# Kernel optimization log

Hardware: AMD Instinct MI355X
Metric: run time of the kernel (lower is better)

Reference implementation:

```python
import jax, jax.numpy as jnp
import numpy as np

B, N, D_MODEL = 4, 4096, 1024
N_HEADS, D_HEAD = 16, 64
NB_FEATURES = int(D_HEAD * np.log(D_HEAD))  # 266, performer default
EPS = 1e-4


def _gaussian_orthogonal_matrix(key, m, d):
    """performer-pytorch gaussian_orthogonal_random_matrix, scaling=0."""
    n_blocks = int(np.ceil(m / d))
    keys = jax.random.split(key, n_blocks + 1)
    blocks = []
    for i in range(n_blocks):
        g = jax.random.normal(keys[i], (d, d), jnp.float32)
        q, _ = jnp.linalg.qr(g)
        blocks.append(q.T)
    mat = jnp.concatenate(blocks, axis=0)[:m]  # [m, d]
    multiplier = jnp.linalg.norm(
        jax.random.normal(keys[-1], (m, d), jnp.float32), axis=1)
    return mat * multiplier[:, None]


def setup_inputs() -> dict:
    key = jax.random.key(0)
    ks = jax.random.split(key, 7)
    s = 1.0 / np.sqrt(D_MODEL)
    x = jax.random.normal(ks[0], (B, N, D_MODEL), jnp.float32)
    Wq = jax.random.normal(ks[1], (D_MODEL, D_MODEL), jnp.float32) * s
    Wk = jax.random.normal(ks[2], (D_MODEL, D_MODEL), jnp.float32) * s
    Wv = jax.random.normal(ks[3], (D_MODEL, D_MODEL), jnp.float32) * s
    Wo = jax.random.normal(ks[4], (D_MODEL, D_MODEL), jnp.float32) * s
    bo = jnp.zeros((D_MODEL,), jnp.float32)
    proj = _gaussian_orthogonal_matrix(ks[5], NB_FEATURES, D_HEAD)
    return {"x": x, "Wq": Wq, "Wk": Wk, "Wv": Wv, "Wo": Wo, "bo": bo,
            "proj": proj}


def _softmax_kernel(data, proj, is_query):
    # data: [b, h, n, d]; proj: [m, d]  (FAVOR+ positive random features)
    ratio = proj.shape[0] ** -0.5
    dn = data.shape[-1] ** -0.25  # data_normalizer
    dash = jnp.einsum('bhnd,md->bhnm', data * dn, proj)
    diag = 0.5 * (dn ** 2) * jnp.sum(data * data, axis=-1, keepdims=True)
    if is_query:
        stab = jnp.max(dash, axis=-1, keepdims=True)
    else:
        stab = jnp.max(dash, axis=(-2, -1), keepdims=True)
    return ratio * (jnp.exp(dash - diag - stab) + EPS)


def reference(x, Wq, Wk, Wv, Wo, bo, proj):
    b, n, _ = x.shape

    def split_heads(t):  # [b,n,D] -> [b,h,n,d]
        return t.reshape(b, n, N_HEADS, D_HEAD).transpose(0, 2, 1, 3)

    q = split_heads(x @ Wq)
    k = split_heads(x @ Wk)
    v = split_heads(x @ Wv)

    qp = _softmax_kernel(q, proj, True)   # [b,h,n,m]
    kp = _softmax_kernel(k, proj, False)  # [b,h,n,m]

    # non-causal linear attention
    k_sum = jnp.sum(kp, axis=2)                                # [b,h,m]
    d_inv = 1.0 / jnp.einsum('bhnm,bhm->bhn', qp, k_sum)       # [b,h,n]
    context = jnp.einsum('bhnm,bhnd->bhmd', kp, v)             # [b,h,m,d]
    out = jnp.einsum('bhnm,bhmd,bhn->bhnd', qp, context, d_inv)

    out = out.transpose(0, 2, 1, 3).reshape(b, n, N_HEADS * D_HEAD)
    return out @ Wo + bo
```

## Files before the change

### kernel.cpp

```cpp
#include <hip/hip_runtime.h>
#include <hip/hip_bf16.h>

typedef unsigned short u16;
typedef unsigned int   u32;
typedef __bf16 bf16x8 __attribute__((ext_vector_type(8)));
typedef float  f32x4  __attribute__((ext_vector_type(4)));
typedef unsigned short u16x8 __attribute__((ext_vector_type(8)));

#define B_    4
#define N_    4096
#define BN_   16384
#define DM_   1024
#define H_    16
#define BH_   64
#define M_    266
#define MP_   288
#define DN_    0.35355339059327373f
#define RATIO_ 0.061313933948496574f
#define EPS_   1e-4f

static __device__ __forceinline__ float b2f(u16 u) {
    union { u32 u; float f; } x; x.u = ((u32)u) << 16; return x.f;
}
static __device__ __forceinline__ u16 f2b(float f) {
    union { float f; u32 u; } x; x.f = f;
    u32 r = x.u + 0x7FFFu + ((x.u >> 16) & 1u);
    return (u16)(r >> 16);
}
static __device__ __forceinline__ u32 ford(float f) {
    u32 u = __float_as_uint(f);
    return (u & 0x80000000u) ? ~u : (u | 0x80000000u);
}
static __device__ __forceinline__ float forddec(u32 u) {
    return (u & 0x80000000u) ? __uint_as_float(u & 0x7FFFFFFFu) : __uint_as_float(~u);
}
static __device__ __forceinline__ f32x4 mfma16(bf16x8 a, bf16x8 b, f32x4 c) {
    return __builtin_amdgcn_mfma_f32_16x16x32_bf16(a, b, c, 0, 0, 0);
}
#define GLOAD16(gp, lp) __builtin_amdgcn_global_load_lds( \
    (const __attribute__((address_space(1))) void*)(gp),  \
    (__attribute__((address_space(3))) void*)(lp), 16, 0, 0)

__global__ __launch_bounds__(256) void pack_all(const float* __restrict__ x, u16* __restrict__ xb,
                                                const float* __restrict__ Wq, const float* __restrict__ Wk,
                                                const float* __restrict__ Wv, const float* __restrict__ Wo,
                                                u16* __restrict__ wT,
                                                const float* __restrict__ proj, u16* __restrict__ projb,
                                                u32* __restrict__ stabk) {
    __shared__ float tile[64][65];
    int bid = blockIdx.x, tid = threadIdx.x;
    if (bid < 16384) {
        int i = (bid * 256 + tid) * 4;
        float4 f = *reinterpret_cast<const float4*>(x + i);
        ushort4 o;
        o.x = f2b(f.x); o.y = f2b(f.y); o.z = f2b(f.z); o.w = f2b(f.w);
        *reinterpret_cast<ushort4*>(xb + i) = o;
    } else if (bid < 16384 + 1024) {
        int u = bid - 16384;
        int i0 = (u & 15) * 64;
        int j0 = (u >> 4) * 64;
        const float* src = (j0 < 1024) ? Wq : (j0 < 2048) ? Wk : (j0 < 3072) ? Wv : Wo;
        int jc = j0 & 1023;
        int tr = tid >> 6, tc = tid & 63;
#pragma unroll
        for (int it = 0; it < 16; ++it) {
            int r = it * 4 + tr;
            tile[r][tc] = src[(size_t)(i0 + r) * 1024 + jc + tc];
        }
        __syncthreads();
#pragma unroll
        for (int it = 0; it < 16; ++it) {
            int r = it * 4 + tr;
            wT[(size_t)(j0 + r) * 1024 + i0 + tc] = f2b(tile[tc][r]);
        }
    } else {
        int i = (bid - 17408) * 256 + tid;
        if (i < MP_ * 64) {
            int m = i >> 6;
            projb[i] = (m < M_) ? f2b(proj[i] * DN_) : (u16)0;
        }
        if (i < BH_) stabk[i] = 0u;
    }
}

template<int OUTF32>
__global__ __launch_bounds__(512, 1) void gemm256(const u16* __restrict__ A, const u16* __restrict__ Bt,
                                                  void* __restrict__ C, const float* __restrict__ bias,
                                                  int Ncols, int nby) {
    __shared__ u16 As[2][256 * 64];
    __shared__ u16 Bs[2][256 * 64];
    constexpr int K = 1024, T = 16;
    int tid = threadIdx.x, lane = tid & 63, wid = tid >> 6;
    int wm = wid >> 2, wn = wid & 3;
    int lr = lane & 15, lk8 = (lane >> 4) * 8;
    int nwg = gridDim.x;
    int wg = ((int)blockIdx.x & 7) * (nwg >> 3) + (int)blockIdx.x / 8;
    int u = wg % (8 * nby), pid = wg / (8 * nby);
    size_t r0 = (size_t)(pid * 8 + (u & 7)) * 256;
    size_t c0 = (size_t)(u / 8) * 256;

    auto stage = [&](int t, int h) {
        int buf = t & 1;
        const u16* src = (h < 2) ? (A + r0 * K) : (Bt + c0 * K);
        u16* dst = (h < 2) ? As[buf] : Bs[buf];
        int rbase = (h & 1) * 128;
        int kt = t * 64;
#pragma unroll
        for (int c = 0; c < 2; ++c) {
            int li0 = rbase * 8 + c * 512 + wid * 64;
            int li = li0 + lane;
            int row = li >> 3, kk = (li & 7) * 8;
            int kks = kk ^ ((row & 7) << 3);
            GLOAD16(&src[(size_t)row * K + kt + kks], (char*)dst + (size_t)li0 * 16);
        }
    };
    auto lda = [&](int buf, int mf, int ks) {
        int row = wm * 128 + mf * 16 + lr;
        return *reinterpret_cast<const bf16x8*>(&As[buf][row * 64 + ((ks * 32 + lk8) ^ ((row & 7) << 3))]);
    };
    auto ldb = [&](int buf, int nf, int ks) {
        int row = wn * 64 + nf * 16 + lr;
        return *reinterpret_cast<const bf16x8*>(&Bs[buf][row * 64 + ((ks * 32 + lk8) ^ ((row & 7) << 3))]);
    };

    f32x4 acc[8][4] = {};
    stage(0, 0); stage(0, 1); stage(0, 2); stage(0, 3);
    stage(1, 2); stage(1, 3); stage(1, 0);
    asm volatile("s_waitcnt vmcnt(6)" ::: "memory");
    __builtin_amdgcn_s_barrier();

#pragma unroll 2
    for (int t = 0; t < T; ++t) {
        const int buf = t & 1;
        bf16x8 av[4][2], aw[4][2], bv[4][2];
#pragma unroll
        for (int mf = 0; mf < 4; ++mf) { av[mf][0] = lda(buf, mf, 0); av[mf][1] = lda(buf, mf, 1); }
#pragma unroll
        for (int nf = 0; nf < 4; ++nf) { bv[nf][0] = ldb(buf, nf, 0); bv[nf][1] = ldb(buf, nf, 1); }
        if (t + 1 < T) stage(t + 1, 1);
        __builtin_amdgcn_s_barrier();
        __builtin_amdgcn_s_setprio(1);
#pragma unroll
        for (int mf = 0; mf < 4; ++mf)
#pragma unroll
            for (int nf = 0; nf < 4; ++nf) {
                acc[mf][nf] = mfma16(av[mf][0], bv[nf][0], acc[mf][nf]);
                acc[mf][nf] = mfma16(av[mf][1], bv[nf][1], acc[mf][nf]);
            }
        __builtin_amdgcn_s_setprio(0);
        __builtin_amdgcn_s_barrier();
#pragma unroll
        for (int mf = 0; mf < 4; ++mf) { aw[mf][0] = lda(buf, 4 + mf, 0); aw[mf][1] = lda(buf, 4 + mf, 1); }
        if (t + 2 < T) stage(t + 2, 2);
        __builtin_amdgcn_s_barrier();
        __builtin_amdgcn_s_setprio(1);
#pragma unroll
        for (int mf = 0; mf < 4; ++mf)
#pragma unroll
            for (int nf = 0; nf < 2; ++nf) {
                acc[4 + mf][nf] = mfma16(aw[mf][0], bv[nf][0], acc[4 + mf][nf]);
                acc[4 + mf][nf] = mfma16(aw[mf][1], bv[nf][1], acc[4 + mf][nf]);
            }
        __builtin_amdgcn_s_setprio(0);
        __builtin_amdgcn_s_barrier();
        if (t + 2 < T) { stage(t + 2, 3); stage(t + 2, 0); }
        __builtin_amdgcn_s_barrier();
        __builtin_amdgcn_s_setprio(1);
#pragma unroll
        for (int mf = 0; mf < 4; ++mf)
#pragma unroll
            for (int nf = 0; nf < 2; ++nf) {
                acc[4 + mf][2 + nf] = mfma16(aw[mf][0], bv[2 + nf][0], acc[4 + mf][2 + nf]);
                acc[4 + mf][2 + nf] = mfma16(aw[mf][1], bv[2 + nf][1], acc[4 + mf][2 + nf]);
            }
        __builtin_amdgcn_s_setprio(0);
        if (t + 2 < T) asm volatile("s_waitcnt vmcnt(6)" ::: "memory");
        else           asm volatile("s_waitcnt vmcnt(0)" ::: "memory");
        __builtin_amdgcn_s_barrier();
    }

    int rq = (lane >> 4) * 4;
#pragma unroll
    for (int mf = 0; mf < 8; ++mf)
#pragma unroll
        for (int nf = 0; nf < 4; ++nf) {
            size_t col = c0 + wn * 64 + nf * 16 + lr;
#pragma unroll
            for (int r = 0; r < 4; ++r) {
                size_t row = r0 + wm * 128 + mf * 16 + rq + r;
                float v = acc[mf][nf][r];
                if (OUTF32) reinterpret_cast<float*>(C)[row * Ncols + col] = v + bias[col];
                else        reinterpret_cast<u16*>(C)[row * Ncols + col] = f2b(v);
            }
        }
}

__global__ __launch_bounds__(256) void dashk_max(const u16* __restrict__ qkv, const u16* __restrict__ projb,
                                                 u32* __restrict__ stabk) {
    __shared__ u16 kt[128 * 64];
    __shared__ float redbuf[4];
    int bh = blockIdx.y, ch = blockIdx.x;
    int b = bh >> 4, h = bh & 15;
    const u16* src = qkv + ((size_t)(b * N_ + ch * 128)) * 3072 + 1024 + h * 64;
    int tid = threadIdx.x;
#pragma unroll
    for (int c = 0; c < 4; ++c) {
        int li = c * 256 + tid;
        int row = li >> 3, kk = (li & 7) * 8;
        *reinterpret_cast<bf16x8*>(&kt[row * 64 + (kk ^ ((row & 7) << 3))]) =
            *reinterpret_cast<const bf16x8*>(&src[(size_t)row * 3072 + kk]);
    }
    __syncthreads();
    int lane = tid & 63, wid = tid >> 6;
    int lr = lane & 15, lk8 = (lane >> 4) * 8;
    float mx = -3.0e38f;
#pragma unroll
    for (int i = 0; i < 2; ++i) {
        int row = wid * 32 + i * 16 + lr;
        bf16x8 a0 = *reinterpret_cast<const bf16x8*>(&kt[row * 64 + (lk8 ^ ((row & 7) << 3))]);
        bf16x8 a1 = *reinterpret_cast<const bf16x8*>(&kt[row * 64 + ((32 + lk8) ^ ((row & 7) << 3))]);
#pragma unroll
        for (int mf = 0; mf < 17; ++mf) {
            f32x4 d = {0.f, 0.f, 0.f, 0.f};
            const u16* pb = projb + (size_t)(mf * 16 + lr) * 64;
            d = mfma16(a0, *reinterpret_cast<const bf16x8*>(pb + lk8), d);
            d = mfma16(a1, *reinterpret_cast<const bf16x8*>(pb + 32 + lk8), d);
            if (mf * 16 + lr < M_)
                mx = fmaxf(mx, fmaxf(fmaxf(d[0], d[1]), fmaxf(d[2], d[3])));
        }
    }
#pragma unroll
    for (int off = 32; off >= 1; off >>= 1) mx = fmaxf(mx, __shfl_xor(mx, off, 64));
    if (lane == 0) redbuf[wid] = mx;
    __syncthreads();
    if (tid == 0) {
        float m = fmaxf(fmaxf(redbuf[0], redbuf[1]), fmaxf(redbuf[2], redbuf[3]));
        atomicMax(&stabk[bh], ford(m));
    }
}

__global__ __launch_bounds__(256) void kp_context(const u16* __restrict__ qkv, const u16* __restrict__ projb,
                                                  const u32* __restrict__ stabk,
                                                  float* __restrict__ ctx_part, float* __restrict__ ksum_part) {
    __shared__ u16 kt[2][64 * 64];
    __shared__ u16 vt[2][64 * 64];
    __shared__ u16 kpT[144 * 64];
    __shared__ float ksum_s[4][144];
    int bh = blockIdx.y, ch = blockIdx.x, mh = blockIdx.z;
    int b = bh >> 4, h = bh & 15;
    int tid = threadIdx.x, lane = tid & 63, wid = tid >> 6;
    int lr = lane & 15, lk8 = (lane >> 4) * 8, rq = (lane >> 4) * 4;
    float stab = forddec(stabk[bh]);
    float ksump[9];
#pragma unroll
    for (int i = 0; i < 9; ++i) ksump[i] = 0.f;
    f32x4 acc[9] = {};
    int drow = wid * 16 + lr;

    auto stage_kv = [&](int sc, int buf) {
        int n0 = ch * 512 + sc * 64;
        const u16* srck = qkv + ((size_t)(b * N_ + n0)) * 3072 + 1024 + h * 64;
        const u16* srcv = srck + 1024;
#pragma unroll
        for (int p = 0; p < 2; ++p) {
            int li0 = (wid * 2 + p) * 64;
            int li = li0 + lane;
            int row = li >> 3, kk = (li & 7) * 8;
            int kks = kk ^ ((row & 7) << 3);
            GLOAD16(&srck[(size_t)row * 3072 + kks], (char*)kt[buf] + (size_t)li0 * 16);
            GLOAD16(&srcv[(size_t)row * 3072 + kks], (char*)vt[buf] + (size_t)li0 * 16);
        }
    };

    stage_kv(0, 0);
    asm volatile("s_waitcnt vmcnt(0)" ::: "memory");
    for (int sc = 0; sc < 8; ++sc) {
        int buf = sc & 1;
        __builtin_amdgcn_s_barrier();
        if (sc < 7) stage_kv(sc + 1, buf ^ 1);
        int n0 = ch * 512 + sc * 64;
        {
            int row = wid * 16 + lr;
            bf16x8 a0 = *reinterpret_cast<const bf16x8*>(&kt[buf][row * 64 + (lk8 ^ ((row & 7) << 3))]);
            bf16x8 a1 = *reinterpret_cast<const bf16x8*>(&kt[buf][row * 64 + ((32 + lk8) ^ ((row & 7) << 3))]);
            float ss = 0.f;
#pragma unroll
            for (int j = 0; j < 8; ++j) {
                float f0 = (float)a0[j]; ss = fmaf(f0, f0, ss);
                float f1 = (float)a1[j]; ss = fmaf(f1, f1, ss);
            }
            ss += __shfl_xor(ss, 16, 64);
            ss += __shfl_xor(ss, 32, 64);
            float dgk[4];
#pragma unroll
            for (int r = 0; r < 4; ++r) dgk[r] = 0.0625f * __shfl(ss, rq + r, 64);
            int c4 = wid * 16 + rq;
#pragma unroll
            for (int mf = 0; mf < 9; ++mf) {
                int mfg = mh * 9 + mf;
                f32x4 d = {0.f, 0.f, 0.f, 0.f};
                const u16* pb = projb + (size_t)(mfg * 16 + lr) * 64;
                d = mfma16(a0, *reinterpret_cast<const bf16x8*>(pb + lk8), d);
                d = mfma16(a1, *reinterpret_cast<const bf16x8*>(pb + 32 + lk8), d);
                int m = mfg * 16 + lr;
                int mloc = mf * 16 + lr;
                bool real = (m < M_);
                ushort4 o;
                float v0 = real ? RATIO_ * (__expf(d[0] - dgk[0] - stab) + EPS_) : 0.f;
                float v1 = real ? RATIO_ * (__expf(d[1] - dgk[1] - stab) + EPS_) : 0.f;
                float v2 = real ? RATIO_ * (__expf(d[2] - dgk[2] - stab) + EPS_) : 0.f;
                float v3 = real ? RATIO_ * (__expf(d[3] - dgk[3] - stab) + EPS_) : 0.f;
                o.x = f2b(v0); o.y = f2b(v1); o.z = f2b(v2); o.w = f2b(v3);
                ksump[mf] += v0 + v1 + v2 + v3;
                *reinterpret_cast<ushort4*>(&kpT[mloc * 64 + (c4 ^ ((mloc & 7) << 3))]) = o;
            }
        }
        asm volatile("s_waitcnt lgkmcnt(0)" ::: "memory");
        __builtin_amdgcn_s_barrier();
        bf16x8 bv[2];
#pragma unroll
        for (int ks = 0; ks < 2; ++ks) {
            union { u16 s[8]; bf16x8 v; } tmp;
#pragma unroll
            for (int j = 0; j < 8; ++j) {
                int n = ks * 32 + lk8 + j;
                tmp.s[j] = vt[buf][n * 64 + ((drow & ~7) ^ ((n & 7) << 3)) + (drow & 7)];
            }
            bv[ks] = tmp.v;
        }
#pragma unroll
        for (int ks = 0; ks < 2; ++ks) {
#pragma unroll
            for (int mf = 0; mf < 9; ++mf) {
                int mrow = mf * 16 + lr;
                bf16x8 av = *reinterpret_cast<const bf16x8*>(
                    &kpT[mrow * 64 + ((ks * 32 + lk8) ^ ((mrow & 7) << 3))]);
                acc[mf] = mfma16(av, bv[ks], acc[mf]);
            }
        }
        if (sc < 7) asm volatile("s_waitcnt vmcnt(0)" ::: "memory");
    }
    size_t basep = ((size_t)ch * BH_ + bh) * MP_;
#pragma unroll
    for (int mf = 0; mf < 9; ++mf) {
#pragma unroll
        for (int r = 0; r < 4; ++r) {
            int m = mh * 144 + mf * 16 + rq + r;
            ctx_part[(basep + m) * 64 + wid * 16 + lr] = acc[mf][r];
        }
    }
#pragma unroll
    for (int mf = 0; mf < 9; ++mf) {
        float v = ksump[mf];
        v += __shfl_xor(v, 16, 64);
        v += __shfl_xor(v, 32, 64);
        if (lane < 16) ksum_s[wid][mf * 16 + lane] = v;
    }
    __syncthreads();
    for (int t = tid; t < 144; t += 256)
        ksum_part[basep + mh * 144 + t] = ksum_s[0][t] + ksum_s[1][t] + ksum_s[2][t] + ksum_s[3][t];
}

__global__ __launch_bounds__(256) void reduce_all(const float* __restrict__ ctx_part,
                                                  const float* __restrict__ ksum_part,
                                                  u16* __restrict__ ctx2, float* __restrict__ ksum) {
    int bid = blockIdx.x, tid = threadIdx.x;
    if (bid < 576) {
        int t = bid * 256 + tid;
        int mo = t % 36;
        int rest = t / 36;
        int d = rest & 63;
        int bh = rest >> 6;
        u16x8 o;
#pragma unroll
        for (int mm = 0; mm < 8; ++mm) {
            int m = mo * 8 + mm;
            float s = 0.f;
#pragma unroll
            for (int c = 0; c < 8; ++c)
                s += ctx_part[(((size_t)c * BH_ + bh) * MP_ + m) * 64 + d];
            o[mm] = f2b(s);
        }
        size_t idx = ((((size_t)bh * 4 + (d >> 4)) * 9 + (mo >> 2)) * 64
                      + (mo & 3) * 16 + (d & 15)) * 8;
        *reinterpret_cast<u16x8*>(ctx2 + idx) = o;
    } else {
        int t = (bid - 576) * 256 + tid;
        float s = 0.f;
#pragma unroll
        for (int c = 0; c < 8; ++c) s += ksum_part[(size_t)c * BH_ * MP_ + t];
        ksum[t] = s;
    }
}

__global__ __launch_bounds__(256) void qp_out(const u16* __restrict__ qkv, const u16* __restrict__ projb,
                                              const float* __restrict__ ksum,
                                              const u16* __restrict__ ctx2, u16* __restrict__ attn) {
    __shared__ u16 qt[64 * 64];
    __shared__ u16 qp_s[64 * 296];
    int bh = blockIdx.y, ch = blockIdx.x;
    int b = bh >> 4, h = bh & 15;
    int tid = threadIdx.x, lane = tid & 63, wid = tid >> 6;
    int lr = lane & 15, lk8 = (lane >> 4) * 8, rq = (lane >> 4) * 4;
    float ksh[18];
#pragma unroll
    for (int mf = 0; mf < 18; ++mf) ksh[mf] = ksum[bh * MP_ + mf * 16 + lr];
    const u16* srcq = qkv + ((size_t)(b * N_ + ch * 128)) * 3072 + h * 64;
    int srow = tid >> 2, skk = (tid & 3) * 16;
    int ssw = (srow & 7) << 3;
    int sd0 = srow * 64 + (skk ^ ssw);
    int sd1 = srow * 64 + ((skk + 8) ^ ssw);
    {
        u16x8 qa = *reinterpret_cast<const u16x8*>(&srcq[(size_t)srow * 3072 + skk]);
        u16x8 qb = *reinterpret_cast<const u16x8*>(&srcq[(size_t)srow * 3072 + skk + 8]);
        *reinterpret_cast<u16x8*>(&qt[sd0]) = qa;
        *reinterpret_cast<u16x8*>(&qt[sd1]) = qb;
    }
    asm volatile("s_waitcnt lgkmcnt(0)" ::: "memory");
    __builtin_amdgcn_s_barrier();
#pragma unroll
    for (int c = 0; c < 2; ++c) {
        int n0 = ch * 128 + c * 64;
        int row = wid * 16 + lr;
        bf16x8 a0 = *reinterpret_cast<const bf16x8*>(&qt[row * 64 + (lk8 ^ ((row & 7) << 3))]);
        bf16x8 a1 = *reinterpret_cast<const bf16x8*>(&qt[row * 64 + ((32 + lk8) ^ ((row & 7) << 3))]);
        u16x8 qa, qb;
        if (c == 0) {
            qa = *reinterpret_cast<const u16x8*>(&srcq[(size_t)(64 + srow) * 3072 + skk]);
            qb = *reinterpret_cast<const u16x8*>(&srcq[(size_t)(64 + srow) * 3072 + skk + 8]);
        }
        float ss = 0.f;
#pragma unroll
        for (int j = 0; j < 8; ++j) {
            float f0 = (float)a0[j]; ss = fmaf(f0, f0, ss);
            float f1 = (float)a1[j]; ss = fmaf(f1, f1, ss);
        }
        ss += __shfl_xor(ss, 16, 64);
        ss += __shfl_xor(ss, 32, 64);
        float dq[4];
#pragma unroll
        for (int r = 0; r < 4; ++r) dq[r] = 0.0625f * __shfl(ss, rq + r, 64);
        f32x4 dall[18];
        float mx[4] = {-3e38f, -3e38f, -3e38f, -3e38f};
#pragma unroll
        for (int mf = 0; mf < 18; ++mf) {
            f32x4 d = {0.f, 0.f, 0.f, 0.f};
            const u16* pb = projb + (size_t)(mf * 16 + lr) * 64;
            d = mfma16(a0, *reinterpret_cast<const bf16x8*>(pb + lk8), d);
            d = mfma16(a1, *reinterpret_cast<const bf16x8*>(pb + 32 + lk8), d);
            dall[mf] = d;
            if (mf * 16 + lr < M_) {
#pragma unroll
                for (int r = 0; r < 4; ++r) mx[r] = fmaxf(mx[r], d[r]);
            }
        }
#pragma unroll
        for (int r = 0; r < 4; ++r) {
#pragma unroll
            for (int off = 1; off < 16; off <<= 1)
                mx[r] = fmaxf(mx[r], __shfl_xor(mx[r], off, 64));
        }
        float den[4] = {0.f, 0.f, 0.f, 0.f};
#pragma unroll
        for (int mf = 0; mf < 18; ++mf) {
            int m = mf * 16 + lr;
            bool real = (m < M_);
#pragma unroll
            for (int r = 0; r < 4; ++r) {
                float qv = real ? RATIO_ * (__expf(dall[mf][r] - dq[r] - mx[r]) + EPS_) : 0.f;
                qp_s[(wid * 16 + rq + r) * 296 + m] = f2b(qv);
                den[r] = fmaf(qv, ksh[mf], den[r]);
            }
        }
        float dinv[4];
#pragma unroll
        for (int r = 0; r < 4; ++r) {
            float s = den[r];
#pragma unroll
            for (int off = 1; off < 16; off <<= 1) s += __shfl_xor(s, off, 64);
            dinv[r] = 1.0f / s;
        }
        __builtin_amdgcn_s_barrier();
        if (c == 0) {
            *reinterpret_cast<u16x8*>(&qt[sd0]) = qa;
            *reinterpret_cast<u16x8*>(&qt[sd1]) = qb;
        }
        bf16x8 aq[9];
#pragma unroll
        for (int ks = 0; ks < 9; ++ks)
            aq[ks] = *reinterpret_cast<const bf16x8*>(&qp_s[(wid * 16 + lr) * 296 + ks * 32 + lk8]);
#pragma unroll
        for (int df = 0; df < 4; ++df) {
            f32x4 o = {0.f, 0.f, 0.f, 0.f};
            const u16* pb = ctx2 + ((((size_t)bh * 4 + df) * 9) * 64 + lane) * 8;
#pragma unroll
            for (int ks = 0; ks < 9; ++ks)
                o = mfma16(aq[ks], *reinterpret_cast<const bf16x8*>(pb + (size_t)ks * 512), o);
#pragma unroll
            for (int r = 0; r < 4; ++r) {
                size_t orow = (size_t)b * N_ + n0 + wid * 16 + rq + r;
                attn[orow * 1024 + h * 64 + df * 16 + lr] = f2b(o[r] * dinv[r]);
            }
        }
        if (c == 0) {
            asm volatile("s_waitcnt lgkmcnt(0)" ::: "memory");
            __builtin_amdgcn_s_barrier();
        }
    }
}

extern "C" void kernel_launch(void* const* d_in, const int* in_sizes, int n_in,
                              void* d_out, int out_size, void* d_ws, size_t ws_size,
                              hipStream_t stream) {
    const float* x    = (const float*)d_in[0];
    const float* Wq   = (const float*)d_in[1];
    const float* Wk   = (const float*)d_in[2];
    const float* Wv   = (const float*)d_in[3];
    const float* Wo   = (const float*)d_in[4];
    const float* bo   = (const float*)d_in[5];
    const float* proj = (const float*)d_in[6];
    char* ws = (char*)d_ws;
    u16*   xb    = (u16*)(ws + 0);
    u16*   wT    = (u16*)(ws + 33554432);
    u16*   qkv   = (u16*)(ws + 41943040);
    u16*   projb = (u16*)(ws + 142606336);
    u32*   stabk = (u32*)(ws + 144740352);
    float* ksum  = (float*)(ws + 144740608);
    u16*   ctx2  = (u16*)(ws + 144814336);
    float* ctxp  = (float*)(ws + 147173632);
    float* ksump = (float*)(ws + 184922368);
    u16*   attn  = (u16*)(ws + 185512192);
    float* out   = (float*)d_out;

    pack_all<<<17480, 256, 0, stream>>>(x, xb, Wq, Wk, Wv, Wo, wT, proj, projb, stabk);
    gemm256<0><<<768, 512, 0, stream>>>(xb, wT, (void*)qkv, nullptr, 3072, 12);
    dashk_max<<<dim3(32, 64), 256, 0, stream>>>(qkv, projb, stabk);
    kp_context<<<dim3(8, 64, 2), 256, 0, stream>>>(qkv, projb, stabk, ctxp, ksump);
    reduce_all<<<648, 256, 0, stream>>>(ctxp, ksump, ctx2, ksum);
    qp_out<<<dim3(32, 64), 256, 0, stream>>>(qkv, projb, ksum, ctx2, attn);
    gemm256<1><<<256, 512, 0, stream>>>(attn, wT + 3072 * 1024, (void*)out, bo, 1024, 4);
}
```

Baseline: 406.5 us.

## Replace global K-max pass with online running-max rescaling in kp_context

Removes the separate dashk_max kernel, which recomputed K·proj over the whole sequence only to find the global stabilizer. kp_context now tracks a per-block running max, rescales its accumulators when the max grows, and reports its local max. reduce_all then rescales the partial contexts and k-sums to a common global max. Because the EPS term cannot be rescaled this way, it is added back analytically: the k-sum gets RATIO·EPS·N, and the context gets RATIO·EPS times the column sum of V, computed from (Σx)·Wv by two new small kernels. This adds an extra barrier per chunk, a weakly parallel vsum kernel, and small numerical differences, since the max includes zero-padded feature columns and the V sum is taken from bf16 x with fp32 Wv.

Result: slower. 428.0 us (+5.3%).

```diff
diff --git a/kernel.cpp b/kernel.cpp
--- a/kernel.cpp
+++ b/kernel.cpp
@@ -27,13 +27,6 @@
     u32 r = x.u + 0x7FFFu + ((x.u >> 16) & 1u);
     return (u16)(r >> 16);
 }
-static __device__ __forceinline__ u32 ford(float f) {
-    u32 u = __float_as_uint(f);
-    return (u & 0x80000000u) ? ~u : (u | 0x80000000u);
-}
-static __device__ __forceinline__ float forddec(u32 u) {
-    return (u & 0x80000000u) ? __uint_as_float(u & 0x7FFFFFFFu) : __uint_as_float(~u);
-}
 static __device__ __forceinline__ f32x4 mfma16(bf16x8 a, bf16x8 b, f32x4 c) {
     return __builtin_amdgcn_mfma_f32_16x16x32_bf16(a, b, c, 0, 0, 0);
 }
@@ -45,8 +38,7 @@
                                                 const float* __restrict__ Wq, const float* __restrict__ Wk,
                                                 const float* __restrict__ Wv, const float* __restrict__ Wo,
                                                 u16* __restrict__ wT,
-                                                const float* __restrict__ proj, u16* __restrict__ projb,
-                                                u32* __restrict__ stabk) {
+                                                const float* __restrict__ proj, u16* __restrict__ projb) {
     __shared__ float tile[64][65];
     int bid = blockIdx.x, tid = threadIdx.x;
     if (bid < 16384) {
@@ -79,8 +71,38 @@
             int m = i >> 6;
             projb[i] = (m < M_) ? f2b(proj[i] * DN_) : (u16)0;
         }
-        if (i < BH_) stabk[i] = 0u;
-    }
+    }
+}
+
+__global__ __launch_bounds__(256) void xsum_kernel(const u16* __restrict__ xb, float* __restrict__ xsump) {
+    int b = blockIdx.x >> 6, nc = blockIdx.x & 63, tid = threadIdx.x;
+    const u16* px = xb + ((size_t)b * N_ + nc * 64) * 1024 + tid * 4;
+    float s0 = 0.f, s1 = 0.f, s2 = 0.f, s3 = 0.f;
+#pragma unroll 4
+    for (int n = 0; n < 64; ++n) {
+        ushort4 v = *reinterpret_cast<const ushort4*>(px + (size_t)n * 1024);
+        s0 += b2f(v.x); s1 += b2f(v.y); s2 += b2f(v.z); s3 += b2f(v.w);
+    }
+    *reinterpret_cast<float4*>(&xsump[(size_t)blockIdx.x * 1024 + tid * 4]) =
+        make_float4(s0, s1, s2, s3);
+}
+
+__global__ __launch_bounds__(256) void vsum_kernel(const float* __restrict__ xsump, const float* __restrict__ Wv,
+                                                   float* __restrict__ vsum) {
+    __shared__ float xs[1024];
+    int b = blockIdx.x >> 2, jc = blockIdx.x & 3, tid = threadIdx.x;
+    for (int i = tid; i < 1024; i += 256) {
+        float s = 0.f;
+#pragma unroll
+        for (int nc = 0; nc < 64; ++nc) s += xsump[((size_t)(b * 64 + nc)) * 1024 + i];
+        xs[i] = s;
+    }
+    __syncthreads();
+    int j = jc * 256 + tid;
+    float acc = 0.f;
+#pragma unroll 8
+    for (int i = 0; i < 1024; ++i) acc = fmaf(xs[i], Wv[(size_t)i * 1024 + j], acc);
+    vsum[b * 1024 + j] = acc;
 }
 
 template<int OUTF32>
@@ -195,66 +217,23 @@
         }
 }
 
-__global__ __launch_bounds__(256) void dashk_max(const u16* __restrict__ qkv, const u16* __restrict__ projb,
-                                                 u32* __restrict__ stabk) {
-    __shared__ u16 kt[128 * 64];
-    __shared__ float redbuf[4];
-    int bh = blockIdx.y, ch = blockIdx.x;
-    int b = bh >> 4, h = bh & 15;
-    const u16* src = qkv + ((size_t)(b * N_ + ch * 128)) * 3072 + 1024 + h * 64;
-    int tid = threadIdx.x;
-#pragma unroll
-    for (int c = 0; c < 4; ++c) {
-        int li = c * 256 + tid;
-        int row = li >> 3, kk = (li & 7) * 8;
-        *reinterpret_cast<bf16x8*>(&kt[row * 64 + (kk ^ ((row & 7) << 3))]) =
-            *reinterpret_cast<const bf16x8*>(&src[(size_t)row * 3072 + kk]);
-    }
-    __syncthreads();
-    int lane = tid & 63, wid = tid >> 6;
-    int lr = lane & 15, lk8 = (lane >> 4) * 8;
-    float mx = -3.0e38f;
-#pragma unroll
-    for (int i = 0; i < 2; ++i) {
-        int row = wid * 32 + i * 16 + lr;
-        bf16x8 a0 = *reinterpret_cast<const bf16x8*>(&kt[row * 64 + (lk8 ^ ((row & 7) << 3))]);
-        bf16x8 a1 = *reinterpret_cast<const bf16x8*>(&kt[row * 64 + ((32 + lk8) ^ ((row & 7) << 3))]);
-#pragma unroll
-        for (int mf = 0; mf < 17; ++mf) {
-            f32x4 d = {0.f, 0.f, 0.f, 0.f};
-            const u16* pb = projb + (size_t)(mf * 16 + lr) * 64;
-            d = mfma16(a0, *reinterpret_cast<const bf16x8*>(pb + lk8), d);
-            d = mfma16(a1, *reinterpret_cast<const bf16x8*>(pb + 32 + lk8), d);
-            if (mf * 16 + lr < M_)
-                mx = fmaxf(mx, fmaxf(fmaxf(d[0], d[1]), fmaxf(d[2], d[3])));
-        }
-    }
-#pragma unroll
-    for (int off = 32; off >= 1; off >>= 1) mx = fmaxf(mx, __shfl_xor(mx, off, 64));
-    if (lane == 0) redbuf[wid] = mx;
-    __syncthreads();
-    if (tid == 0) {
-        float m = fmaxf(fmaxf(redbuf[0], redbuf[1]), fmaxf(redbuf[2], redbuf[3]));
-        atomicMax(&stabk[bh], ford(m));
-    }
-}
-
 __global__ __launch_bounds__(256) void kp_context(const u16* __restrict__ qkv, const u16* __restrict__ projb,
-                                                  const u32* __restrict__ stabk,
-                                                  float* __restrict__ ctx_part, float* __restrict__ ksum_part) {
+                                                  float* __restrict__ ctx_part, float* __restrict__ ksum_part,
+                                                  float* __restrict__ lmax) {
     __shared__ u16 kt[2][64 * 64];
     __shared__ u16 vt[2][64 * 64];
     __shared__ u16 kpT[144 * 64];
     __shared__ float ksum_s[4][144];
+    __shared__ float redbuf[4];
     int bh = blockIdx.y, ch = blockIdx.x, mh = blockIdx.z;
     int b = bh >> 4, h = bh & 15;
     int tid = threadIdx.x, lane = tid & 63, wid = tid >> 6;
     int lr = lane & 15, lk8 = (lane >> 4) * 8, rq = (lane >> 4) * 4;
-    float stab = forddec(stabk[bh]);
     float ksump[9];
 #pragma unroll
     for (int i = 0; i < 9; ++i) ksump[i] = 0.f;
     f32x4 acc[9] = {};
+    float m_run = -3.0e38f;
     int drow = wid * 16 + lr;
 
     auto stage_kv = [&](int sc, int buf) {
@@ -278,42 +257,63 @@
         int buf = sc & 1;
         __builtin_amdgcn_s_barrier();
         if (sc < 7) stage_kv(sc + 1, buf ^ 1);
-        int n0 = ch * 512 + sc * 64;
-        {
-            int row = wid * 16 + lr;
-            bf16x8 a0 = *reinterpret_cast<const bf16x8*>(&kt[buf][row * 64 + (lk8 ^ ((row & 7) << 3))]);
-            bf16x8 a1 = *reinterpret_cast<const bf16x8*>(&kt[buf][row * 64 + ((32 + lk8) ^ ((row & 7) << 3))]);
-            float ss = 0.f;
-#pragma unroll
-            for (int j = 0; j < 8; ++j) {
-                float f0 = (float)a0[j]; ss = fmaf(f0, f0, ss);
-                float f1 = (float)a1[j]; ss = fmaf(f1, f1, ss);
-            }
-            ss += __shfl_xor(ss, 16, 64);
-            ss += __shfl_xor(ss, 32, 64);
-            float dgk[4];
-#pragma unroll
-            for (int r = 0; r < 4; ++r) dgk[r] = 0.0625f * __shfl(ss, rq + r, 64);
-            int c4 = wid * 16 + rq;
+        int row = wid * 16 + lr;
+        bf16x8 a0 = *reinterpret_cast<const bf16x8*>(&kt[buf][row * 64 + (lk8 ^ ((row & 7) << 3))]);
+        bf16x8 a1 = *reinterpret_cast<const bf16x8*>(&kt[buf][row * 64 + ((32 + lk8) ^ ((row & 7) << 3))]);
+        float ss = 0.f;
+#pragma unroll
+        for (int j = 0; j < 8; ++j) {
+            float f0 = (float)a0[j]; ss = fmaf(f0, f0, ss);
+            float f1 = (float)a1[j]; ss = fmaf(f1, f1, ss);
+        }
+        ss += __shfl_xor(ss, 16, 64);
+        ss += __shfl_xor(ss, 32, 64);
+        float dgk[4];
+#pragma unroll
+        for (int r = 0; r < 4; ++r) dgk[r] = 0.0625f * __shfl(ss, rq + r, 64);
+        f32x4 dall[9];
+        float tmax = -3.0e38f;
+#pragma unroll
+        for (int mf = 0; mf < 9; ++mf) {
+            int mfg = mh * 9 + mf;
+            f32x4 d = {0.f, 0.f, 0.f, 0.f};
+            const u16* pb = projb + (size_t)(mfg * 16 + lr) * 64;
+            d = mfma16(a0, *reinterpret_cast<const bf16x8*>(pb + lk8), d);
+            d = mfma16(a1, *reinterpret_cast<const bf16x8*>(pb + 32 + lk8), d);
+            dall[mf] = d;
+            tmax = fmaxf(tmax, fmaxf(fmaxf(d[0], d[1]), fmaxf(d[2], d[3])));
+        }
+#pragma unroll
+        for (int off = 1; off < 64; off <<= 1) tmax = fmaxf(tmax, __shfl_xor(tmax, off, 64));
+        if (lane == 0) redbuf[wid] = tmax;
+        asm volatile("s_waitcnt lgkmcnt(0)" ::: "memory");
+        __builtin_amdgcn_s_barrier();
+        float bmax = fmaxf(fmaxf(redbuf[0], redbuf[1]), fmaxf(redbuf[2], redbuf[3]));
+        if (bmax > m_run) {
+            float c = __expf(m_run - bmax);
 #pragma unroll
             for (int mf = 0; mf < 9; ++mf) {
-                int mfg = mh * 9 + mf;
-                f32x4 d = {0.f, 0.f, 0.f, 0.f};
-                const u16* pb = projb + (size_t)(mfg * 16 + lr) * 64;
-                d = mfma16(a0, *reinterpret_cast<const bf16x8*>(pb + lk8), d);
-                d = mfma16(a1, *reinterpret_cast<const bf16x8*>(pb + 32 + lk8), d);
-                int m = mfg * 16 + lr;
-                int mloc = mf * 16 + lr;
-                bool real = (m < M_);
-                ushort4 o;
-                float v0 = real ? RATIO_ * (__expf(d[0] - dgk[0] - stab) + EPS_) : 0.f;
-                float v1 = real ? RATIO_ * (__expf(d[1] - dgk[1] - stab) + EPS_) : 0.f;
-                float v2 = real ? RATIO_ * (__expf(d[2] - dgk[2] - stab) + EPS_) : 0.f;
-                float v3 = real ? RATIO_ * (__expf(d[3] - dgk[3] - stab) + EPS_) : 0.f;
-                o.x = f2b(v0); o.y = f2b(v1); o.z = f2b(v2); o.w = f2b(v3);
-                ksump[mf] += v0 + v1 + v2 + v3;
-                *reinterpret_cast<ushort4*>(&kpT[mloc * 64 + (c4 ^ ((mloc & 7) << 3))]) = o;
-            }
+#pragma unroll
+                for (int r = 0; r < 4; ++r) acc[mf][r] *= c;
+                ksump[mf] *= c;
+            }
+            m_run = bmax;
+        }
+        int c4 = wid * 16 + rq;
+#pragma unroll
+        for (int mf = 0; mf < 9; ++mf) {
+            int mfg = mh * 9 + mf;
+            int m = mfg * 16 + lr;
+            int mloc = mf * 16 + lr;
+            bool real = (m < M_);
+            float v0 = real ? RATIO_ * __expf(dall[mf][0] - dgk[0] - m_run) : 0.f;
+            float v1 = real ? RATIO_ * __expf(dall[mf][1] - dgk[1] - m_run) : 0.f;
+            float v2 = real ? RATIO_ * __expf(dall[mf][2] - dgk[2] - m_run) : 0.f;
+            float v3 = real ? RATIO_ * __expf(dall[mf][3] - dgk[3] - m_run) : 0.f;
+            ushort4 o;
+            o.x = f2b(v0); o.y = f2b(v1); o.z = f2b(v2); o.w = f2b(v3);
+            ksump[mf] += v0 + v1 + v2 + v3;
+            *reinterpret_cast<ushort4*>(&kpT[mloc * 64 + (c4 ^ ((mloc & 7) << 3))]) = o;
         }
         asm volatile("s_waitcnt lgkmcnt(0)" ::: "memory");
         __builtin_amdgcn_s_barrier();
@@ -359,10 +359,13 @@
     __syncthreads();
     for (int t = tid; t < 144; t += 256)
         ksum_part[basep + mh * 144 + t] = ksum_s[0][t] + ksum_s[1][t] + ksum_s[2][t] + ksum_s[3][t];
+    if (tid == 0) lmax[bh * 16 + ch * 2 + mh] = m_run;
 }
 
 __global__ __launch_bounds__(256) void reduce_all(const float* __restrict__ ctx_part,
                                                   const float* __restrict__ ksum_part,
+                                                  const float* __restrict__ lmax,
+                                                  const float* __restrict__ vsum,
                                                   u16* __restrict__ ctx2, float* __restrict__ ksum) {
     int bid = blockIdx.x, tid = threadIdx.x;
     if (bid < 576) {
@@ -371,6 +374,15 @@
         int rest = t / 36;
         int d = rest & 63;
         int bh = rest >> 6;
+        int b = bh >> 4, h = bh & 15;
+        int mh = (mo >= 18);
+        float gm = -3.0e38f;
+#pragma unroll
+        for (int c = 0; c < 16; ++c) gm = fmaxf(gm, lmax[bh * 16 + c]);
+        float scl[8];
+#pragma unroll
+        for (int c = 0; c < 8; ++c) scl[c] = __expf(lmax[bh * 16 + c * 2 + mh] - gm);
+        float ve = RATIO_ * EPS_ * vsum[b * 1024 + h * 64 + d];
         u16x8 o;
 #pragma unroll
         for (int mm = 0; mm < 8; ++mm) {
@@ -378,7 +390,8 @@
             float s = 0.f;
 #pragma unroll
             for (int c = 0; c < 8; ++c)
-                s += ctx_part[(((size_t)c * BH_ + bh) * MP_ + m) * 64 + d];
+                s += scl[c] * ctx_part[(((size_t)c * BH_ + bh) * MP_ + m) * 64 + d];
+            if (m < M_) s += ve;
             o[mm] = f2b(s);
         }
         size_t idx = ((((size_t)bh * 4 + (d >> 4)) * 9 + (mo >> 2)) * 64
@@ -386,9 +399,16 @@
         *reinterpret_cast<u16x8*>(ctx2 + idx) = o;
     } else {
         int t = (bid - 576) * 256 + tid;
+        int bh = t / MP_, m = t % MP_;
+        int mh = (m >= 144);
+        float gm = -3.0e38f;
+#pragma unroll
+        for (int c = 0; c < 16; ++c) gm = fmaxf(gm, lmax[bh * 16 + c]);
         float s = 0.f;
 #pragma unroll
-        for (int c = 0; c < 8; ++c) s += ksum_part[(size_t)c * BH_ * MP_ + t];
+        for (int c = 0; c < 8; ++c)
+            s += __expf(lmax[bh * 16 + c * 2 + mh] - gm) * ksum_part[(size_t)c * BH_ * MP_ + t];
+        if (m < M_) s += RATIO_ * EPS_ * (float)N_;
         ksum[t] = s;
     }
 }
@@ -524,7 +544,9 @@
     u16*   wT    = (u16*)(ws + 33554432);
     u16*   qkv   = (u16*)(ws + 41943040);
     u16*   projb = (u16*)(ws + 142606336);
-    u32*   stabk = (u32*)(ws + 144740352);
+    float* xsump = (float*)(ws + 142643200);
+    float* vsum  = (float*)(ws + 143691776);
+    float* lmax  = (float*)(ws + 143708160);
     float* ksum  = (float*)(ws + 144740608);
     u16*   ctx2  = (u16*)(ws + 144814336);
     float* ctxp  = (float*)(ws + 147173632);
@@ -532,11 +554,12 @@
     u16*   attn  = (u16*)(ws + 185512192);
     float* out   = (float*)d_out;
 
-    pack_all<<<17480, 256, 0, stream>>>(x, xb, Wq, Wk, Wv, Wo, wT, proj, projb, stabk);
+    pack_all<<<17480, 256, 0, stream>>>(x, xb, Wq, Wk, Wv, Wo, wT, proj, projb);
+    xsum_kernel<<<256, 256, 0, stream>>>(xb, xsump);
+    vsum_kernel<<<16, 256, 0, stream>>>(xsump, Wv, vsum);
     gemm256<0><<<768, 512, 0, stream>>>(xb, wT, (void*)qkv, nullptr, 3072, 12);
-    dashk_max<<<dim3(32, 64), 256, 0, stream>>>(qkv, projb, stabk);
-    kp_context<<<dim3(8, 64, 2), 256, 0, stream>>>(qkv, projb, stabk, ctxp, ksump);
-    reduce_all<<<648, 256, 0, stream>>>(ctxp, ksump, ctx2, ksum);
+    kp_context<<<dim3(8, 64, 2), 256, 0, stream>>>(qkv, projb, ctxp, ksump, lmax);
+    reduce_all<<<648, 256, 0, stream>>>(ctxp, ksump, lmax, vsum, ctx2, ksum);
     qp_out<<<dim3(32, 64), 256, 0, stream>>>(qkv, projb, ksum, ctx2, attn);
     gemm256<1><<<256, 512, 0, stream>>>(attn, wT + 3072 * 1024, (void*)out, bo, 1024, 4);
 }
```

## Merge kp_context feature halves into one 512-thread block sharing K/V tiles

Applied to the files above, without the earlier changes.

The kp_context kernel used to launch two blocks per chunk (one per half of the random features), each loading the same K and V tiles. It now launches one 512-thread block per chunk in which two groups of four waves each handle one feature half and share a single staged K/V tile. This halves global K/V traffic and the staging work for this kernel, but doubles the kpT and ksum shared-memory footprint per block and halves the number of blocks, which may reduce occupancy and latency hiding.

After: 511.1 us. 25.7% more time.

```diff
diff --git a/kernel.cpp b/kernel.cpp
--- a/kernel.cpp
+++ b/kernel.cpp
@@ -239,37 +239,35 @@
     }
 }
 
-__global__ __launch_bounds__(256) void kp_context(const u16* __restrict__ qkv, const u16* __restrict__ projb,
-                                                  const u32* __restrict__ stabk,
-                                                  float* __restrict__ ctx_part, float* __restrict__ ksum_part) {
+__global__ __launch_bounds__(512, 4) void kp_context(const u16* __restrict__ qkv, const u16* __restrict__ projb,
+                                                     const u32* __restrict__ stabk,
+                                                     float* __restrict__ ctx_part, float* __restrict__ ksum_part) {
     __shared__ u16 kt[2][64 * 64];
     __shared__ u16 vt[2][64 * 64];
-    __shared__ u16 kpT[144 * 64];
-    __shared__ float ksum_s[4][144];
-    int bh = blockIdx.y, ch = blockIdx.x, mh = blockIdx.z;
+    __shared__ u16 kpT[MP_ * 64];
+    __shared__ float ksum_s[4][MP_];
+    int bh = blockIdx.y, ch = blockIdx.x;
     int b = bh >> 4, h = bh & 15;
     int tid = threadIdx.x, lane = tid & 63, wid = tid >> 6;
+    int grp = wid >> 2, wid4 = wid & 3;
     int lr = lane & 15, lk8 = (lane >> 4) * 8, rq = (lane >> 4) * 4;
     float stab = forddec(stabk[bh]);
     float ksump[9];
 #pragma unroll
     for (int i = 0; i < 9; ++i) ksump[i] = 0.f;
     f32x4 acc[9] = {};
-    int drow = wid * 16 + lr;
+    int drow = wid4 * 16 + lr;
 
     auto stage_kv = [&](int sc, int buf) {
         int n0 = ch * 512 + sc * 64;
         const u16* srck = qkv + ((size_t)(b * N_ + n0)) * 3072 + 1024 + h * 64;
         const u16* srcv = srck + 1024;
-#pragma unroll
-        for (int p = 0; p < 2; ++p) {
-            int li0 = (wid * 2 + p) * 64;
-            int li = li0 + lane;
-            int row = li >> 3, kk = (li & 7) * 8;
-            int kks = kk ^ ((row & 7) << 3);
-            GLOAD16(&srck[(size_t)row * 3072 + kks], (char*)kt[buf] + (size_t)li0 * 16);
-            GLOAD16(&srcv[(size_t)row * 3072 + kks], (char*)vt[buf] + (size_t)li0 * 16);
-        }
+        int li0 = wid * 64;
+        int li = li0 + lane;
+        int row = li >> 3, kk = (li & 7) * 8;
+        int kks = kk ^ ((row & 7) << 3);
+        GLOAD16(&srck[(size_t)row * 3072 + kks], (char*)kt[buf] + (size_t)li0 * 16);
+        GLOAD16(&srcv[(size_t)row * 3072 + kks], (char*)vt[buf] + (size_t)li0 * 16);
     };
 
     stage_kv(0, 0);
@@ -278,9 +276,8 @@
         int buf = sc & 1;
         __builtin_amdgcn_s_barrier();
         if (sc < 7) stage_kv(sc + 1, buf ^ 1);
-        int n0 = ch * 512 + sc * 64;
         {
-            int row = wid * 16 + lr;
+            int row = wid4 * 16 + lr;
             bf16x8 a0 = *reinterpret_cast<const bf16x8*>(&kt[buf][row * 64 + (lk8 ^ ((row & 7) << 3))]);
             bf16x8 a1 = *reinterpret_cast<const bf16x8*>(&kt[buf][row * 64 + ((32 + lk8) ^ ((row & 7) << 3))]);
             float ss = 0.f;
@@ -294,16 +291,15 @@
             float dgk[4];
 #pragma unroll
             for (int r = 0; r < 4; ++r) dgk[r] = 0.0625f * __shfl(ss, rq + r, 64);
-            int c4 = wid * 16 + rq;
+            int c4 = wid4 * 16 + rq;
 #pragma unroll
             for (int mf = 0; mf < 9; ++mf) {
-                int mfg = mh * 9 + mf;
+                int mfg = grp * 9 + mf;
                 f32x4 d = {0.f, 0.f, 0.f, 0.f};
                 const u16* pb = projb + (size_t)(mfg * 16 + lr) * 64;
                 d = mfma16(a0, *reinterpret_cast<const bf16x8*>(pb + lk8), d);
                 d = mfma16(a1, *reinterpret_cast<const bf16x8*>(pb + 32 + lk8), d);
                 int m = mfg * 16 + lr;
-                int mloc = mf * 16 + lr;
                 bool real = (m < M_);
                 ushort4 o;
                 float v0 = real ? RATIO_ * (__expf(d[0] - dgk[0] - stab) + EPS_) : 0.f;
@@ -312,7 +308,7 @@
                 float v3 = real ? RATIO_ * (__expf(d[3] - dgk[3] - stab) + EPS_) : 0.f;
                 o.x = f2b(v0); o.y = f2b(v1); o.z = f2b(v2); o.w = f2b(v3);
                 ksump[mf] += v0 + v1 + v2 + v3;
-                *reinterpret_cast<ushort4*>(&kpT[mloc * 64 + (c4 ^ ((mloc & 7) << 3))]) = o;
+                *reinterpret_cast<ushort4*>(&kpT[m * 64 + (c4 ^ ((m & 7) << 3))]) = o;
             }
         }
         asm volatile("s_waitcnt lgkmcnt(0)" ::: "memory");
@@ -332,7 +328,7 @@
         for (int ks = 0; ks < 2; ++ks) {
 #pragma unroll
             for (int mf = 0; mf < 9; ++mf) {
-                int mrow = mf * 16 + lr;
+                int mrow = (grp * 9 + mf) * 16 + lr;
                 bf16x8 av = *reinterpret_cast<const bf16x8*>(
                     &kpT[mrow * 64 + ((ks * 32 + lk8) ^ ((mrow & 7) << 3))]);
                 acc[mf] = mfma16(av, bv[ks], acc[mf]);
@@ -345,8 +341,8 @@
     for (int mf = 0; mf < 9; ++mf) {
 #pragma unroll
         for (int r = 0; r < 4; ++r) {
-            int m = mh * 144 + mf * 16 + rq + r;
-            ctx_part[(basep + m) * 64 + wid * 16 + lr] = acc[mf][r];
+            int m = (grp * 9 + mf) * 16 + rq + r;
+            ctx_part[(basep + m) * 64 + wid4 * 16 + lr] = acc[mf][r];
         }
     }
 #pragma unroll
@@ -354,11 +350,11 @@
         float v = ksump[mf];
         v += __shfl_xor(v, 16, 64);
         v += __shfl_xor(v, 32, 64);
-        if (lane < 16) ksum_s[wid][mf * 16 + lane] = v;
+        if (lane < 16) ksum_s[wid4][(grp * 9 + mf) * 16 + lane] = v;
     }
     __syncthreads();
-    for (int t = tid; t < 144; t += 256)
-        ksum_part[basep + mh * 144 + t] = ksum_s[0][t] + ksum_s[1][t] + ksum_s[2][t] + ksum_s[3][t];
+    for (int t = tid; t < MP_; t += 512)
+        ksum_part[basep + t] = ksum_s[0][t] + ksum_s[1][t] + ksum_s[2][t] + ksum_s[3][t];
 }
 
 __global__ __launch_bounds__(256) void reduce_all(const float* __restrict__ ctx_part,
@@ -535,7 +531,7 @@
     pack_all<<<17480, 256, 0, stream>>>(x, xb, Wq, Wk, Wv, Wo, wT, proj, projb, stabk);
     gemm256<0><<<768, 512, 0, stream>>>(xb, wT, (void*)qkv, nullptr, 3072, 12);
     dashk_max<<<dim3(32, 64), 256, 0, stream>>>(qkv, projb, stabk);
-    kp_context<<<dim3(8, 64, 2), 256, 0, stream>>>(qkv, projb, stabk, ctxp, ksump);
+    kp_context<<<dim3(8, 64), 512, 0, stream>>>(qkv, projb, stabk, ctxp, ksump);
     reduce_all<<<648, 256, 0, stream>>>(ctxp, ksump, ctx2, ksum);
     qp_out<<<dim3(32, 64), 256, 0, stream>>>(qkv, projb, ksum, ctx2, attn);
     gemm256<1><<<256, 512, 0, stream>>>(attn, wT + 3072 * 1024, (void*)out, bo, 1024, 4);
```
